# Kernel optimization log

Hardware: AMD Instinct MI355X
Metric: run time of the kernel (lower is better)

Reference implementation:

```python
import jax, jax.numpy as jnp
import numpy as np

SC = np.float32(np.sqrt(0.5))


def _reflect_idx(l, m):
    # symmetric-extension gather indices for a length-l axis padded by m each side
    x = np.arange(-m, l + m, dtype=np.float64)
    minx, maxx = -0.5, l - 0.5
    rng = maxx - minx
    mod = np.fmod(x - minx, 2.0 * rng)
    mod = np.where(mod < 0, mod + 2.0 * rng, mod)
    out = np.where(mod >= rng, 2.0 * rng - mod, mod) + minx
    return out.astype(np.int32)


def _conv_h(X, h):
    # true 'valid' convolution (filter flipped, as np.convolve) along H of (N,C,H,W)
    k = h.shape[0]
    w = jnp.flip(h).reshape(1, 1, k, 1).astype(X.dtype)
    N, C, H, W = X.shape
    y = jax.lax.conv_general_dilated(X.reshape(N * C, 1, H, W), w, (1, 1), 'VALID',
                                     dimension_numbers=('NCHW', 'OIHW', 'NCHW'))
    return y.reshape(N, C, -1, W)


def colfilter(X, h):
    # odd-tap filter along rows (H) with symmetric padding, output same H
    m = h.shape[0] // 2
    xe = _reflect_idx(X.shape[2], m)
    return _conv_h(X[:, :, xe], h)


def rowfilter(X, h):
    return colfilter(X.transpose(0, 1, 3, 2), h).transpose(0, 1, 3, 2)


def colifilt(X, ha, hb, highpass):
    # Polyphase form of dtcwt's colifilt: four phase outputs interleaved into 2*H rows.
    N, C, r, W = X.shape
    m = ha.shape[0]
    m2 = m // 2
    xe = _reflect_idx(r, m2)  # len r + m
    hao, hae = ha[0::2], ha[1::2]
    hbo, hbe = hb[0::2], hb[1::2]
    if m2 % 2 == 0:
        t = np.arange(3, r + m, 2)
        off = 2
    else:
        t = np.arange(2, r + m - 1, 2)
        off = 0
    # highpass pairs have sum(ha*hb) < 0 -> swapped quarter-sample phases
    ta, tb = (t - 1, t) if highpass else (t, t - 1)
    Xb = X[:, :, xe[tb - off]]
    Xa = X[:, :, xe[ta - off]]
    Xb2 = X[:, :, xe[tb]] if off else Xb
    Xa2 = X[:, :, xe[ta]] if off else Xa
    y0 = _conv_h(Xb, hao)
    y1 = _conv_h(Xa, hbo)
    y2 = _conv_h(Xb2, hae)
    y3 = _conv_h(Xa2, hbe)
    Y = jnp.stack([y0, y1, y2, y3], axis=3)  # (N,C,r/2,4,W)
    return Y.reshape(N, C, 2 * r, W)


def rowifilt(X, ha, hb, highpass):
    return colifilt(X.transpose(0, 1, 3, 2), ha, hb, highpass).transpose(0, 1, 3, 2)


def c2q(w1, w2):
    # complex orientation pair (N,C,h,w,2) -> real quad image (N,C,2h,2w)
    w1r, w1i = w1[..., 0], w1[..., 1]
    w2r, w2i = w2[..., 0], w2[..., 1]
    x1 = (w1r + w2r) * SC  # top-left
    x2 = (w1i + w2i) * SC  # top-right
    x3 = (w1i - w2i) * SC  # bottom-left
    x4 = (w2r - w1r) * SC  # bottom-right
    N, C, H, W = x1.shape
    top = jnp.stack([x1, x2], axis=-1).reshape(N, C, H, 2 * W)
    bot = jnp.stack([x3, x4], axis=-1).reshape(N, C, H, 2 * W)
    return jnp.stack([top, bot], axis=3).reshape(N, C, 2 * H, 2 * W)


def _bands(yh):
    lh = c2q(yh[:, :, 0], yh[:, :, 5])
    hl = c2q(yh[:, :, 2], yh[:, :, 3])
    hh = c2q(yh[:, :, 1], yh[:, :, 4])
    return lh, hl, hh


def _crop(ll, ref):
    if ll.shape[2] != ref.shape[2]:
        ll = ll[:, :, 1:-1]
    if ll.shape[3] != ref.shape[3]:
        ll = ll[:, :, :, 1:-1]
    return ll


def _inv_j2plus(ll, yh, g0a, g0b, g1a, g1b):
    lh, hl, hh = _bands(yh)
    ll = _crop(ll, lh)
    y1 = colifilt(ll, g0b, g0a, False) + colifilt(lh, g1b, g1a, True)
    y2 = colifilt(hl, g0b, g0a, False) + colifilt(hh, g1b, g1a, True)
    return rowifilt(y1, g0b, g0a, False) + rowifilt(y2, g1b, g1a, True)


def _inv_j1(ll, yh, g0o, g1o):
    lh, hl, hh = _bands(yh)
    ll = _crop(ll, lh)
    y1 = colfilter(ll, g0o) + colfilter(lh, g1o)
    y2 = colfilter(hl, g0o) + colfilter(hh, g1o)
    return rowfilter(y1, g0o) + rowfilter(y2, g1o)


def _filters():
    # near_sym_a (5,7)-tap biorthogonal synthesis filters
    g0o = np.array([-3.0, -15.0, 73.0, 170.0, 73.0, -15.0, -3.0]) / 280.0
    g1o = np.array([-1.0, -5.0, 12.0, -5.0, -1.0]) / 20.0
    # qshift_06 10-tap quarter-shift filters
    h0a = np.array([0.03516384, 0.0, -0.08832942, 0.23389032, 0.76027237,
                    0.58751830, 0.0, -0.11430184, 0.0, 0.0])
    g0b = h0a
    g0a = h0a[::-1]
    g1a = h0a * np.array([1.0, -1.0] * 5)
    g1b = g1a[::-1]
    f32 = lambda a: jnp.asarray(np.ascontiguousarray(a), dtype=jnp.float32)
    return f32(g0o), f32(g1o), f32(g0a), f32(g0b), f32(g1a), f32(g1b)


def setup_inputs():
    key = jax.random.key(0)
    k1, k2, k3, k4 = jax.random.split(key, 4)
    N, C = 4, 64
    yl = jax.random.normal(k1, (N, C, 64, 64), dtype=jnp.float32)
    yh1 = jax.random.normal(k2, (N, C, 6, 128, 128, 2), dtype=jnp.float32)
    yh2 = jax.random.normal(k3, (N, C, 6, 64, 64, 2), dtype=jnp.float32)
    yh3 = jax.random.normal(k4, (N, C, 6, 32, 32, 2), dtype=jnp.float32)
    g0o, g1o, g0a, g0b, g1a, g1b = _filters()
    return {"yl": yl, "yh1": yh1, "yh2": yh2, "yh3": yh3,
            "g0o": g0o, "g1o": g1o, "g0a": g0a, "g0b": g0b, "g1a": g1a, "g1b": g1b}


def reference(yl, yh1, yh2, yh3, g0o, g1o, g0a, g0b, g1a, g1b):
    ll = _inv_j2plus(yl, yh3, g0a, g0b, g1a, g1b)   # 64 -> 128
    ll = _inv_j2plus(ll, yh2, g0a, g0b, g1a, g1b)   # 128 -> 256
    return _inv_j1(ll, yh1, g0o, g1o)               # 256 -> 256
```

## Files before the change

kernel.cpp:

```cpp
#include <hip/hip_runtime.h>

#define SC 0.70710678118654752440f

__device__ __forceinline__ int reflFull(int p, int n) {
    int x = max(p, ~p);
    return min(x, 2 * n - 1 - x);
}

__device__ __forceinline__ int pairRefl(int t, int NP, bool& sw) {
    int x = max(t, ~t);
    int tp = min(x, 2 * NP - 1 - x);
    sw = (tp != t);
    return tp;
}

__device__ __forceinline__ constexpr int cflIdx(int s, int k) {
    return (s == 0) ? 8 - 2 * k : (s == 1) ? 1 + 2 * k : (s == 2) ? 9 - 2 * k : 2 * k;
}
__device__ __forceinline__ constexpr int cfhIdx(int s, int k) {
    return (s == 0) ? 1 + 2 * k : (s == 1) ? 8 - 2 * k : (s == 2) ? 2 * k : 9 - 2 * k;
}

__device__ __forceinline__ float4 f4fma(float c, float4 a, float4 acc) {
    return make_float4(fmaf(c, a.x, acc.x), fmaf(c, a.y, acc.y),
                       fmaf(c, a.z, acc.z), fmaf(c, a.w, acc.w));
}
__device__ __forceinline__ float4 f4sel(bool sw, float4 a, float4 b) {
    return sw ? a : b;
}

struct Band4 { float4 e05, o05, e23, o23, e14, o14; };

__device__ __forceinline__ Band4 loadBands4(const float* __restrict__ bp, int HW2,
                                            int boff, bool sw) {
    float4 B0 = *(const float4*)(bp + 0 * HW2 + boff);
    float4 B1 = *(const float4*)(bp + 1 * HW2 + boff);
    float4 B2 = *(const float4*)(bp + 2 * HW2 + boff);
    float4 B3 = *(const float4*)(bp + 3 * HW2 + boff);
    float4 B4 = *(const float4*)(bp + 4 * HW2 + boff);
    float4 B5 = *(const float4*)(bp + 5 * HW2 + boff);
    float4 ve05 = {B0.x + B5.x, B0.y + B5.y, B0.z + B5.z, B0.w + B5.w};
    float4 vo05 = {B0.y - B5.y, B5.x - B0.x, B0.w - B5.w, B5.z - B0.z};
    float4 ve23 = {B2.x + B3.x, B2.y + B3.y, B2.z + B3.z, B2.w + B3.w};
    float4 vo23 = {B2.y - B3.y, B3.x - B2.x, B2.w - B3.w, B3.z - B2.z};
    float4 ve14 = {B1.x + B4.x, B1.y + B4.y, B1.z + B4.z, B1.w + B4.w};
    float4 vo14 = {B1.y - B4.y, B4.x - B1.x, B1.w - B4.w, B4.z - B1.z};
    Band4 r;
    r.e05 = f4sel(sw, vo05, ve05);  r.o05 = f4sel(sw, ve05, vo05);
    r.e23 = f4sel(sw, vo23, ve23);  r.o23 = f4sel(sw, ve23, vo23);
    r.e14 = f4sel(sw, vo14, ve14);  r.o14 = f4sel(sw, ve14, vo14);
    return r;
}

template <int N> struct Log2 { static constexpr int v = 1 + Log2<N / 2>::v; };
template <> struct Log2<1> { static constexpr int v = 0; };

template <int H, int W>
__global__ __launch_bounds__(256) void j2_fused(
        const float* __restrict__ ll, const float* __restrict__ yh,
        const float* __restrict__ g0b, const float* __restrict__ g1a,
        float* __restrict__ out) {
    constexpr int LOGW = Log2<W>::v;
    constexpr int U4 = W / 2, LOGU4 = LOGW - 1;
    constexpr int QI = 256 / U4;
    constexpr int TI = 4 * QI;
    constexpr int r = 2 * H, C2 = 2 * W, COUT = 4 * W, LOGC2 = LOGW + 1;
    constexpr int HW2 = H * W * 2;
    __shared__ float sY1[TI][C2];
    __shared__ float sY2[TI][C2];

    const int tid = threadIdx.x;
    const int nc = blockIdx.y;
    const int q0 = blockIdx.x * QI;
    const float* llp = ll + (size_t)nc * r * C2;
    const float* bp  = yh + (size_t)nc * 6 * HW2;

    float G0[10], G1[10];
#pragma unroll
    for (int i = 0; i < 10; ++i) { G0[i] = g0b[i]; G1[i] = g1a[i]; }

    {
        int u4 = tid & (U4 - 1);
        int qq = tid >> LOGU4;
        int q = q0 + qq;
        float4 A1[4], A1b[4], A2[4];
#pragma unroll
        for (int s = 0; s < 4; ++s) {
            A1[s] = {0, 0, 0, 0}; A1b[s] = {0, 0, 0, 0}; A2[s] = {0, 0, 0, 0};
        }
#pragma unroll
        for (int k = 0; k < 5; ++k) {
            int t = q + k - 2;
            int pe = reflFull(2 * t, r);
            int po = reflFull(2 * t + 1, r);
            float4 lle = *(const float4*)(llp + ((pe << LOGC2) + 4 * u4));
            float4 llo = *(const float4*)(llp + ((po << LOGC2) + 4 * u4));
            bool sw; int tp = pairRefl(t, H, sw);
            int boff = (tp << (LOGW + 1)) + 4 * u4;
            Band4 B = loadBands4(bp, HW2, boff, sw);
#pragma unroll
            for (int s = 0; s < 4; ++s) {
                float4 lv  = (s & 1) ? llo   : lle;
                float4 v05 = (s & 1) ? B.e05 : B.o05;
                float4 v23 = (s & 1) ? B.o23 : B.e23;
                float4 v14 = (s & 1) ? B.e14 : B.o14;
                float c0 = G0[cflIdx(s, k)];
                float c1 = G1[cfhIdx(s, k)];
                A1[s]  = f4fma(c0, lv,  A1[s]);
                A1b[s] = f4fma(c1, v05, A1b[s]);
                A2[s]  = f4fma(c0, v23, f4fma(c1, v14, A2[s]));
            }
        }
#pragma unroll
        for (int s = 0; s < 4; ++s) {
            float4 w1 = f4fma(SC, A1b[s], A1[s]);
            float4 w2 = {SC * A2[s].x, SC * A2[s].y, SC * A2[s].z, SC * A2[s].w};
            *(float4*)&sY1[4 * qq + s][4 * u4] = w1;
            *(float4*)&sY2[4 * qq + s][4 * u4] = w2;
        }
    }
    __syncthreads();

    float* op = out + (size_t)nc * (4 * H) * COUT;
#pragma unroll
    for (int v = 0; v < (TI * W) / 256; ++v) {
        int lin = v * 256 + tid;
        int qc = lin & (W - 1);
        int il = lin >> LOGW;
        float e1[5], o1[5], e2[5], o2[5];
#pragma unroll
        for (int m = 0; m < 5; ++m) {
            int t = qc + m - 2;
            bool sw; int tp = pairRefl(t, W, sw);
            float2 f1 = *(const float2*)&sY1[il][2 * tp];
            float2 f2 = *(const float2*)&sY2[il][2 * tp];
            e1[m] = sw ? f1.y : f1.x;  o1[m] = sw ? f1.x : f1.y;
            e2[m] = sw ? f2.y : f2.x;  o2[m] = sw ? f2.x : f2.y;
        }
        float acc[4];
#pragma unroll
        for (int s = 0; s < 4; ++s) {
            float a = 0.f;
#pragma unroll
            for (int k = 0; k < 5; ++k) {
                float v1 = (s & 1) ? o1[k] : e1[k];
                float v2 = (s & 1) ? e2[k] : o2[k];
                a = fmaf(G0[cflIdx(s, k)], v1, a);
                a = fmaf(G1[cfhIdx(s, k)], v2, a);
            }
            acc[s] = a;
        }
        int grow = 4 * q0 + il;
        *(float4*)(op + (size_t)grow * COUT + 4 * qc) =
            make_float4(acc[0], acc[1], acc[2], acc[3]);
    }
}

template <int H, int W>
__global__ __launch_bounds__(256) void j1_fused(
        const float* __restrict__ ll, const float* __restrict__ yh,
        const float* __restrict__ g0o, const float* __restrict__ g1o,
        float* __restrict__ out) {
    constexpr int LOGW = Log2<W>::v;
    constexpr int U4 = W / 2, LOGU4 = LOGW - 1;
    constexpr int QI = 256 / U4;
    constexpr int TI = 4 * QI;
    constexpr int r = 2 * H, c = 2 * W, LOGC2 = LOGW + 1;
    constexpr int HW2 = H * W * 2;
    __shared__ float sY1[TI][c];
    __shared__ float sY2[TI][c];

    const int tid = threadIdx.x;
    const int nc = blockIdx.y;
    const int qi0 = blockIdx.x * QI;
    const float* llp = ll + (size_t)nc * r * c;
    const float* bp  = yh + (size_t)nc * 6 * HW2;

    float g0f[7], g1f[5];
#pragma unroll
    for (int k = 0; k < 7; ++k) g0f[k] = g0o[6 - k];
#pragma unroll
    for (int k = 0; k < 5; ++k) g1f[k] = g1o[4 - k];

    {
        int u4 = tid & (U4 - 1);
        int qq = tid >> LOGU4;
        int qi = qi0 + qq;
        float4 A1[4], A1b[4], A2[4];
#pragma unroll
        for (int s = 0; s < 4; ++s) {
            A1[s] = {0, 0, 0, 0}; A1b[s] = {0, 0, 0, 0}; A2[s] = {0, 0, 0, 0};
        }
#pragma unroll
        for (int rr = 0; rr < 10; ++rr) {
            int p = reflFull(4 * qi - 3 + rr, r);
            float4 v = *(const float4*)(llp + ((p << LOGC2) + 4 * u4));
#pragma unroll
            for (int di = 0; di < 4; ++di) {
                int k = rr - di;
                if (k >= 0 && k <= 6) A1[di] = f4fma(g0f[k], v, A1[di]);
            }
        }
#pragma unroll
        for (int tr = 0; tr < 6; ++tr) {
            int t = 2 * qi - 2 + tr;
            bool sw; int tp = pairRefl(t, H, sw);
            int boff = (tp << (LOGW + 1)) + 4 * u4;
            Band4 B = loadBands4(bp, HW2, boff, sw);
#pragma unroll
            for (int di = 0; di < 4; ++di) {
                int k1e = 2 * tr - di - 2;
                int k1o = k1e + 1;
                int k0e = 2 * tr - di - 1;
                int k0o = k0e + 1;
                if (k1e >= 0 && k1e <= 4) {
                    A1b[di] = f4fma(g1f[k1e], B.e05, A1b[di]);
                    A2[di]  = f4fma(g1f[k1e], B.e14, A2[di]);
                }
                if (k1o >= 0 && k1o <= 4) {
                    A1b[di] = f4fma(g1f[k1o], B.o05, A1b[di]);
                    A2[di]  = f4fma(g1f[k1o], B.o14, A2[di]);
                }
                if (k0e >= 0 && k0e <= 6) A2[di] = f4fma(g0f[k0e], B.e23, A2[di]);
                if (k0o >= 0 && k0o <= 6) A2[di] = f4fma(g0f[k0o], B.o23, A2[di]);
            }
        }
#pragma unroll
        for (int di = 0; di < 4; ++di) {
            float4 w1 = f4fma(SC, A1b[di], A1[di]);
            float4 w2 = {SC * A2[di].x, SC * A2[di].y, SC * A2[di].z, SC * A2[di].w};
            *(float4*)&sY1[4 * qq + di][4 * u4] = w1;
            *(float4*)&sY2[4 * qq + di][4 * u4] = w2;
        }
    }
    __syncthreads();

    float* op = out + (size_t)nc * r * c;
#pragma unroll
    for (int v = 0; v < (TI * (W / 2)) / 256; ++v) {
        int lin = v * 256 + tid;
        int uq = lin & (W / 2 - 1);
        int il = lin >> (LOGW - 1);
        float e1[6], o1[6], e2[6], o2[6];
#pragma unroll
        for (int m = 0; m < 6; ++m) {
            int t = 2 * uq - 2 + m;
            bool sw; int tp = pairRefl(t, W, sw);
            float2 f1 = *(const float2*)&sY1[il][2 * tp];
            float2 f2 = *(const float2*)&sY2[il][2 * tp];
            e1[m] = sw ? f1.y : f1.x;  o1[m] = sw ? f1.x : f1.y;
            e2[m] = sw ? f2.y : f2.x;  o2[m] = sw ? f2.x : f2.y;
        }
        float acc[4];
#pragma unroll
        for (int s = 0; s < 4; ++s) {
            float a = 0.f;
#pragma unroll
            for (int k = 0; k < 7; ++k) {
                int rel = s + k + 1;
                int m = rel >> 1;
                a = fmaf(g0f[k], (rel & 1) ? o1[m] : e1[m], a);
            }
#pragma unroll
            for (int k = 0; k < 5; ++k) {
                int rel = s + k + 2;
                int m = rel >> 1;
                a = fmaf(g1f[k], (rel & 1) ? o2[m] : e2[m], a);
            }
            acc[s] = a;
        }
        int grow = 4 * qi0 + il;
        *(float4*)(op + (size_t)grow * c + 4 * uq) =
            make_float4(acc[0], acc[1], acc[2], acc[3]);
    }
}

extern "C" void kernel_launch(void* const* d_in, const int* in_sizes, int n_in,
                              void* d_out, int out_size, void* d_ws, size_t ws_size,
                              hipStream_t stream) {
    const float* yl  = (const float*)d_in[0];
    const float* yh1 = (const float*)d_in[1];
    const float* yh2 = (const float*)d_in[2];
    const float* yh3 = (const float*)d_in[3];
    const float* g0o = (const float*)d_in[4];
    const float* g1o = (const float*)d_in[5];
    const float* g0b = (const float*)d_in[7];
    const float* g1a = (const float*)d_in[8];
    float* out = (float*)d_out;

    const int NC = 256;
    char* ws = (char*)d_ws;
    float* llA = (float*)ws;
    float* llB = (float*)(ws + ((size_t)16 << 20));

    j2_fused<32, 32><<<dim3(2, NC), 256, 0, stream>>>(yl, yh3, g0b, g1a, llA);
    j2_fused<64, 64><<<dim3(8, NC), 256, 0, stream>>>(llA, yh2, g0b, g1a, llB);
    j1_fused<128, 128><<<dim3(16, NC), 256, 0, stream>>>(llB, yh1, g0o, g1o, out);
}
```

Before: 117.5 us.

## Store intermediate lowpass images in fp16 and interleave shared buffers

The two intermediate lowpass workspace buffers between the three inverse-DTCWT stages are now written and read as _Float16 instead of float32, with conversion helpers for loads and stores. This halves the global memory traffic for those intermediates in a bandwidth-bound pipeline. The two shared-memory staging arrays are also merged into one float4 array, so each tap is a single LDS read. The cost is lower intermediate precision, which could exceed the accuracy tolerance.

```diff
diff --git a/kernel.cpp b/kernel.cpp
--- a/kernel.cpp
+++ b/kernel.cpp
@@ -1,6 +1,25 @@
 #include <hip/hip_runtime.h>
 
 #define SC 0.70710678118654752440f
+
+typedef _Float16 h4v __attribute__((ext_vector_type(4)));
+
+__device__ __forceinline__ float4 ld4(const float* __restrict__ p) {
+    return *(const float4*)p;
+}
+__device__ __forceinline__ float4 ld4(const _Float16* __restrict__ p) {
+    h4v h = *(const h4v*)p;
+    return make_float4((float)h[0], (float)h[1], (float)h[2], (float)h[3]);
+}
+__device__ __forceinline__ void st4(float* __restrict__ p, float4 v) {
+    *(float4*)p = v;
+}
+__device__ __forceinline__ void st4(_Float16* __restrict__ p, float4 v) {
+    h4v h;
+    h[0] = (_Float16)v.x; h[1] = (_Float16)v.y;
+    h[2] = (_Float16)v.z; h[3] = (_Float16)v.w;
+    *(h4v*)p = h;
+}
 
 __device__ __forceinline__ int reflFull(int p, int n) {
     int x = max(p, ~p);
@@ -55,24 +74,23 @@
 template <int N> struct Log2 { static constexpr int v = 1 + Log2<N / 2>::v; };
 template <> struct Log2<1> { static constexpr int v = 0; };
 
-template <int H, int W>
+template <int H, int W, typename TIn, typename TOut>
 __global__ __launch_bounds__(256) void j2_fused(
-        const float* __restrict__ ll, const float* __restrict__ yh,
+        const TIn* __restrict__ ll, const float* __restrict__ yh,
         const float* __restrict__ g0b, const float* __restrict__ g1a,
-        float* __restrict__ out) {
+        TOut* __restrict__ out) {
     constexpr int LOGW = Log2<W>::v;
     constexpr int U4 = W / 2, LOGU4 = LOGW - 1;
     constexpr int QI = 256 / U4;
     constexpr int TI = 4 * QI;
     constexpr int r = 2 * H, C2 = 2 * W, COUT = 4 * W, LOGC2 = LOGW + 1;
     constexpr int HW2 = H * W * 2;
-    __shared__ float sY1[TI][C2];
-    __shared__ float sY2[TI][C2];
+    __shared__ float4 sY[TI][W];
 
     const int tid = threadIdx.x;
     const int nc = blockIdx.y;
     const int q0 = blockIdx.x * QI;
-    const float* llp = ll + (size_t)nc * r * C2;
+    const TIn* llp = ll + (size_t)nc * r * C2;
     const float* bp  = yh + (size_t)nc * 6 * HW2;
 
     float G0[10], G1[10];
@@ -93,8 +111,8 @@
             int t = q + k - 2;
             int pe = reflFull(2 * t, r);
             int po = reflFull(2 * t + 1, r);
-            float4 lle = *(const float4*)(llp + ((pe << LOGC2) + 4 * u4));
-            float4 llo = *(const float4*)(llp + ((po << LOGC2) + 4 * u4));
+            float4 lle = ld4(llp + ((pe << LOGC2) + 4 * u4));
+            float4 llo = ld4(llp + ((po << LOGC2) + 4 * u4));
             bool sw; int tp = pairRefl(t, H, sw);
             int boff = (tp << (LOGW + 1)) + 4 * u4;
             Band4 B = loadBands4(bp, HW2, boff, sw);
@@ -115,13 +133,13 @@
         for (int s = 0; s < 4; ++s) {
             float4 w1 = f4fma(SC, A1b[s], A1[s]);
             float4 w2 = {SC * A2[s].x, SC * A2[s].y, SC * A2[s].z, SC * A2[s].w};
-            *(float4*)&sY1[4 * qq + s][4 * u4] = w1;
-            *(float4*)&sY2[4 * qq + s][4 * u4] = w2;
+            sY[4 * qq + s][2 * u4]     = make_float4(w1.x, w1.y, w2.x, w2.y);
+            sY[4 * qq + s][2 * u4 + 1] = make_float4(w1.z, w1.w, w2.z, w2.w);
         }
     }
     __syncthreads();
 
-    float* op = out + (size_t)nc * (4 * H) * COUT;
+    TOut* op = out + (size_t)nc * (4 * H) * COUT;
 #pragma unroll
     for (int v = 0; v < (TI * W) / 256; ++v) {
         int lin = v * 256 + tid;
@@ -132,10 +150,9 @@
         for (int m = 0; m < 5; ++m) {
             int t = qc + m - 2;
             bool sw; int tp = pairRefl(t, W, sw);
-            float2 f1 = *(const float2*)&sY1[il][2 * tp];
-            float2 f2 = *(const float2*)&sY2[il][2 * tp];
-            e1[m] = sw ? f1.y : f1.x;  o1[m] = sw ? f1.x : f1.y;
-            e2[m] = sw ? f2.y : f2.x;  o2[m] = sw ? f2.x : f2.y;
+            float4 F = sY[il][tp];
+            e1[m] = sw ? F.y : F.x;  o1[m] = sw ? F.x : F.y;
+            e2[m] = sw ? F.w : F.z;  o2[m] = sw ? F.z : F.w;
         }
         float acc[4];
 #pragma unroll
@@ -151,14 +168,14 @@
             acc[s] = a;
         }
         int grow = 4 * q0 + il;
-        *(float4*)(op + (size_t)grow * COUT + 4 * qc) =
-            make_float4(acc[0], acc[1], acc[2], acc[3]);
+        st4(op + (size_t)grow * COUT + 4 * qc,
+            make_float4(acc[0], acc[1], acc[2], acc[3]));
     }
 }
 
-template <int H, int W>
+template <int H, int W, typename TIn>
 __global__ __launch_bounds__(256) void j1_fused(
-        const float* __restrict__ ll, const float* __restrict__ yh,
+        const TIn* __restrict__ ll, const float* __restrict__ yh,
         const float* __restrict__ g0o, const float* __restrict__ g1o,
         float* __restrict__ out) {
     constexpr int LOGW = Log2<W>::v;
@@ -167,13 +184,12 @@
     constexpr int TI = 4 * QI;
     constexpr int r = 2 * H, c = 2 * W, LOGC2 = LOGW + 1;
     constexpr int HW2 = H * W * 2;
-    __shared__ float sY1[TI][c];
-    __shared__ float sY2[TI][c];
+    __shared__ float4 sY[TI][W];
 
     const int tid = threadIdx.x;
     const int nc = blockIdx.y;
     const int qi0 = blockIdx.x * QI;
-    const float* llp = ll + (size_t)nc * r * c;
+    const TIn* llp = ll + (size_t)nc * r * c;
     const float* bp  = yh + (size_t)nc * 6 * HW2;
 
     float g0f[7], g1f[5];
@@ -194,7 +210,7 @@
 #pragma unroll
         for (int rr = 0; rr < 10; ++rr) {
             int p = reflFull(4 * qi - 3 + rr, r);
-            float4 v = *(const float4*)(llp + ((p << LOGC2) + 4 * u4));
+            float4 v = ld4(llp + ((p << LOGC2) + 4 * u4));
 #pragma unroll
             for (int di = 0; di < 4; ++di) {
                 int k = rr - di;
@@ -229,8 +245,8 @@
         for (int di = 0; di < 4; ++di) {
             float4 w1 = f4fma(SC, A1b[di], A1[di]);
             float4 w2 = {SC * A2[di].x, SC * A2[di].y, SC * A2[di].z, SC * A2[di].w};
-            *(float4*)&sY1[4 * qq + di][4 * u4] = w1;
-            *(float4*)&sY2[4 * qq + di][4 * u4] = w2;
+            sY[4 * qq + di][2 * u4]     = make_float4(w1.x, w1.y, w2.x, w2.y);
+            sY[4 * qq + di][2 * u4 + 1] = make_float4(w1.z, w1.w, w2.z, w2.w);
         }
     }
     __syncthreads();
@@ -246,10 +262,9 @@
         for (int m = 0; m < 6; ++m) {
             int t = 2 * uq - 2 + m;
             bool sw; int tp = pairRefl(t, W, sw);
-            float2 f1 = *(const float2*)&sY1[il][2 * tp];
-            float2 f2 = *(const float2*)&sY2[il][2 * tp];
-            e1[m] = sw ? f1.y : f1.x;  o1[m] = sw ? f1.x : f1.y;
-            e2[m] = sw ? f2.y : f2.x;  o2[m] = sw ? f2.x : f2.y;
+            float4 F = sY[il][tp];
+            e1[m] = sw ? F.y : F.x;  o1[m] = sw ? F.x : F.y;
+            e2[m] = sw ? F.w : F.z;  o2[m] = sw ? F.z : F.w;
         }
         float acc[4];
 #pragma unroll
@@ -290,10 +305,13 @@
 
     const int NC = 256;
     char* ws = (char*)d_ws;
-    float* llA = (float*)ws;
-    float* llB = (float*)(ws + ((size_t)16 << 20));
-
-    j2_fused<32, 32><<<dim3(2, NC), 256, 0, stream>>>(yl, yh3, g0b, g1a, llA);
-    j2_fused<64, 64><<<dim3(8, NC), 256, 0, stream>>>(llA, yh2, g0b, g1a, llB);
-    j1_fused<128, 128><<<dim3(16, NC), 256, 0, stream>>>(llB, yh1, g0o, g1o, out);
-}
+    _Float16* llA = (_Float16*)ws;
+    _Float16* llB = (_Float16*)(ws + ((size_t)16 << 20));
+
+    j2_fused<32, 32, float, _Float16><<<dim3(2, NC), 256, 0, stream>>>(
+        yl, yh3, g0b, g1a, llA);
+    j2_fused<64, 64, _Float16, _Float16><<<dim3(8, NC), 256, 0, stream>>>(
+        llA, yh2, g0b, g1a, llB);
+    j1_fused<128, 128, _Float16><<<dim3(16, NC), 256, 0, stream>>>(
+        llB, yh1, g0o, g1o, out);
+}
```

After: 100.7 us. 14.3% less time.
